# Kernel optimization log

Measured on AMD Instinct MI355X. Metric: run time of the kernel, lower is better.

Reference implementation:

```python
import jax, jax.numpy as jnp
import numpy as np

N_NODES = 50000


def _gin_conv(x, src, dst, w1, b1, w2, b2):
    # sum-aggregate neighbor features: agg[i] = sum_{(j->i) in E} x[j]
    agg = jax.ops.segment_sum(x[src], dst, num_segments=N_NODES)
    h = x + agg  # eps = 0 (PyG GINConv default, not trainable)
    h = jnp.maximum(h @ w1 + b1, 0.0) @ w2 + b2
    return h


def setup_inputs() -> dict:
    key = jax.random.key(0)
    ks = jax.random.split(key, 10)
    d_in, d_h, d_out = 128, 256, 2
    E = 600000
    x = jax.random.normal(ks[0], (N_NODES, d_in), dtype=jnp.float32)
    edge_index = jax.random.randint(ks[1], (2, E), 0, N_NODES, dtype=jnp.int64)
    s = lambda k, sh: jax.random.normal(k, sh, dtype=jnp.float32) * (1.0 / np.sqrt(sh[0]))
    return {
        "x": x,
        "edge_index": edge_index,
        "w1": s(ks[2], (d_in, d_h)), "b1": jnp.zeros((d_h,), jnp.float32),
        "w2": s(ks[3], (d_h, d_h)), "b2": jnp.zeros((d_h,), jnp.float32),
        "w3": s(ks[4], (d_h, d_h)), "b3": jnp.zeros((d_h,), jnp.float32),
        "w4": s(ks[5], (d_h, d_out)), "b4": jnp.zeros((d_out,), jnp.float32),
    }


def reference(x, edge_index, w1, b1, w2, b2, w3, b3, w4, b4):
    src, dst = edge_index[0], edge_index[1]
    h = _gin_conv(x, src, dst, w1, b1, w2, b2)
    h = jnp.maximum(h, 0.0)  # F.relu between the two GINConv layers
    h = _gin_conv(h, src, dst, w3, b3, w4, b4)
    return jax.nn.log_softmax(h, axis=1)
```

## Files before the change

kernel.cpp:

```cpp
#include <hip/hip_runtime.h>
#include <hip/hip_bf16.h>


typedef __attribute__((ext_vector_type(8))) short bf16x8;
typedef __attribute__((ext_vector_type(4))) float f32x4;

static __device__ __forceinline__ unsigned short f2bf(float f) {
    unsigned int u = __float_as_uint(f);
    unsigned int r = (u + 0x7fffu + ((u >> 16) & 1u)) >> 16;
    return (unsigned short)r;
}
static __device__ __forceinline__ float bf2f(unsigned short s) {
    return __uint_as_float(((unsigned int)s) << 16);
}
static __device__ __forceinline__ float bflo(unsigned int u) {
    return __uint_as_float(u << 16);
}
static __device__ __forceinline__ float bfhi(unsigned int u) {
    return __uint_as_float(u & 0xffff0000u);
}

#define S1 136
#define S2 264

__global__ __launch_bounds__(256) void prep_kernel(
    const float* __restrict__ x, short* __restrict__ x_bf,
    const float* __restrict__ w1, const float* __restrict__ w2, const float* __restrict__ w3,
    short* __restrict__ w1t, short* __restrict__ w2t, short* __restrict__ w3t,
    const int* __restrict__ dst, int* __restrict__ deg,
    int M, int E, int cB)
{
    const int b = blockIdx.x;
    const int t = threadIdx.x;
    if (b < cB) {
        const int i = b * 256 + t;
        const int n4 = M * 32;
        if (i >= n4) return;
        const float4 v = *(const float4*)(x + (size_t)i * 4);
        ushort4 o;
        o.x = f2bf(v.x); o.y = f2bf(v.y); o.z = f2bf(v.z); o.w = f2bf(v.w);
        *(ushort4*)(x_bf + (size_t)i * 4) = o;
        return;
    }
    if (b < cB + 192) {
        const int tb = b - cB;
        const int z = tb >> 6;
        const int rem = tb & 63;
        const int kb = rem & 7;
        const int nb = rem >> 3;
        const float* in; short* outb; int K, ostride;
        if (z == 0)      { in = w1; outb = w1t; K = 128; ostride = S1; }
        else if (z == 1) { in = w2; outb = w2t; K = 256; ostride = S2; }
        else             { in = w3; outb = w3t; K = 256; ostride = S2; }
        const int N = 256;
        const int k0 = kb * 32;
        if (k0 >= K) return;
        const int n0 = nb * 32;
        __shared__ float tile[32][33];
        const int tx = t & 31;
        const int ty = t >> 5;
        #pragma unroll
        for (int i = 0; i < 4; ++i)
            tile[ty + 8 * i][tx] = in[(size_t)(k0 + ty + 8 * i) * N + n0 + tx];
        __syncthreads();
        #pragma unroll
        for (int i = 0; i < 4; ++i)
            outb[(size_t)(n0 + ty + 8 * i) * ostride + k0 + tx] = (short)f2bf(tile[tx][ty + 8 * i]);
        return;
    }
    const int e = (b - cB - 192) * 256 + t;
    if (e < E) atomicAdd(&deg[dst[e]], 1);
}

__global__ __launch_bounds__(256) void block_sum_kernel(
    const int* __restrict__ deg, int* __restrict__ bsum, int M)
{
    const int b = blockIdx.x, t = threadIdx.x;
    const int idx = b * 1024 + t * 4;
    int s = 0;
    if (idx + 3 < M) {
        const int4 v = *(const int4*)(deg + idx);
        s = v.x + v.y + v.z + v.w;
    } else {
        #pragma unroll
        for (int i = 0; i < 4; ++i) if (idx + i < M) s += deg[idx + i];
    }
    #pragma unroll
    for (int off = 32; off > 0; off >>= 1) s += __shfl_down(s, off);
    __shared__ int ws[4];
    if ((t & 63) == 0) ws[t >> 6] = s;
    __syncthreads();
    if (t == 0) bsum[b] = ws[0] + ws[1] + ws[2] + ws[3];
}

__global__ __launch_bounds__(256) void scan_blocks2_kernel(
    const int* __restrict__ deg, const int* __restrict__ bsum,
    int* __restrict__ rowptr, int* __restrict__ cur, int M, int E, int nB)
{
    const int b = blockIdx.x, t = threadIdx.x;
    __shared__ int sboff;
    if (t < 64) {
        const int v = (t < nB) ? bsum[t] : 0;
        int inc = v;
        #pragma unroll
        for (int off = 1; off < 64; off <<= 1) {
            const int u = __shfl_up(inc, off);
            if (t >= off) inc += u;
        }
        const int prev = __shfl(inc, (b == 0) ? 0 : (b - 1));
        if (t == 0) sboff = (b == 0) ? 0 : prev;
    }
    const int idx = b * 1024 + t * 4;
    int4 d = make_int4(0, 0, 0, 0);
    if (idx + 3 < M) {
        d = *(const int4*)(deg + idx);
    } else {
        if (idx + 0 < M) d.x = deg[idx + 0];
        if (idx + 1 < M) d.y = deg[idx + 1];
        if (idx + 2 < M) d.z = deg[idx + 2];
        if (idx + 3 < M) d.w = deg[idx + 3];
    }
    const int tot = d.x + d.y + d.z + d.w;
    const int lane = t & 63, wid = t >> 6;
    int inc = tot;
    #pragma unroll
    for (int off = 1; off < 64; off <<= 1) {
        const int u = __shfl_up(inc, off);
        if (lane >= off) inc += u;
    }
    __shared__ int wsum[4];
    if (lane == 63) wsum[wid] = inc;
    __syncthreads();
    int woff = 0;
    #pragma unroll
    for (int w = 0; w < 4; ++w) if (w < wid) woff += wsum[w];
    int p = sboff + woff + (inc - tot);
    if (idx + 0 < M) { rowptr[idx + 0] = p; cur[idx + 0] = p; } p += d.x;
    if (idx + 1 < M) { rowptr[idx + 1] = p; cur[idx + 1] = p; } p += d.y;
    if (idx + 2 < M) { rowptr[idx + 2] = p; cur[idx + 2] = p; } p += d.z;
    if (idx + 3 < M) { rowptr[idx + 3] = p; cur[idx + 3] = p; }
    if (b == 0 && t == 0) rowptr[M] = E;
}

__global__ __launch_bounds__(256) void fill_kernel(
    const int* __restrict__ src, const int* __restrict__ dst,
    int* __restrict__ cur, int* __restrict__ srcs, int E)
{
    const int e = blockIdx.x * 256 + threadIdx.x;
    if (e >= E) return;
    const int p = atomicAdd(&cur[dst[e]], 1);
    srcs[p] = src[e];
}

__global__ __launch_bounds__(256) void gather_add_d128(
    const short* __restrict__ feat,
    const int* __restrict__ rowptr, const int* __restrict__ srcs,
    short* __restrict__ outb, int M)
{
    const int row = blockIdx.x * 4 + (threadIdx.x >> 6);
    if (row >= M) return;
    const int lane = threadIdx.x & 63;
    const int qt = lane >> 4;
    const int o = (lane & 15) * 8;
    float a[8];
    #pragma unroll
    for (int k = 0; k < 8; ++k) a[k] = 0.f;
    if (qt == 0) {
        const uint4 u = *(const uint4*)(feat + (size_t)row * 128 + o);
        a[0] = bflo(u.x); a[1] = bfhi(u.x); a[2] = bflo(u.y); a[3] = bfhi(u.y);
        a[4] = bflo(u.z); a[5] = bfhi(u.z); a[6] = bflo(u.w); a[7] = bfhi(u.w);
    }
    const int jb = rowptr[row], je = rowptr[row + 1];
    int j = jb;
    for (; j + 8 <= je; j += 8) {
        uint4 v[2];
        #pragma unroll
        for (int t = 0; t < 2; ++t) {
            const int s = srcs[j + 4 * t + qt];
            v[t] = *(const uint4*)(feat + (size_t)s * 128 + o);
        }
        #pragma unroll
        for (int t = 0; t < 2; ++t) {
            a[0] += bflo(v[t].x); a[1] += bfhi(v[t].x);
            a[2] += bflo(v[t].y); a[3] += bfhi(v[t].y);
            a[4] += bflo(v[t].z); a[5] += bfhi(v[t].z);
            a[6] += bflo(v[t].w); a[7] += bfhi(v[t].w);
        }
    }
    if (j + 4 <= je) {
        const int s = srcs[j + qt];
        const uint4 v = *(const uint4*)(feat + (size_t)s * 128 + o);
        a[0] += bflo(v.x); a[1] += bfhi(v.x); a[2] += bflo(v.y); a[3] += bfhi(v.y);
        a[4] += bflo(v.z); a[5] += bfhi(v.z); a[6] += bflo(v.w); a[7] += bfhi(v.w);
        j += 4;
    }
    if (j + qt < je) {
        const int s = srcs[j + qt];
        const uint4 v = *(const uint4*)(feat + (size_t)s * 128 + o);
        a[0] += bflo(v.x); a[1] += bfhi(v.x); a[2] += bflo(v.y); a[3] += bfhi(v.y);
        a[4] += bflo(v.z); a[5] += bfhi(v.z); a[6] += bflo(v.w); a[7] += bfhi(v.w);
    }
    #pragma unroll
    for (int k = 0; k < 8; ++k) {
        a[k] += __shfl_down(a[k], 16);
        a[k] += __shfl_down(a[k], 32);
    }
    if (qt == 0) {
        uint4 up;
        up.x = (unsigned int)f2bf(a[0]) | ((unsigned int)f2bf(a[1]) << 16);
        up.y = (unsigned int)f2bf(a[2]) | ((unsigned int)f2bf(a[3]) << 16);
        up.z = (unsigned int)f2bf(a[4]) | ((unsigned int)f2bf(a[5]) << 16);
        up.w = (unsigned int)f2bf(a[6]) | ((unsigned int)f2bf(a[7]) << 16);
        *(uint4*)(outb + (size_t)row * S1 + o) = up;
    }
}

__global__ __launch_bounds__(256) void gather_add_d256(
    const short* __restrict__ feat,
    const int* __restrict__ rowptr, const int* __restrict__ srcs,
    short* __restrict__ outb, int M)
{
    const int row = blockIdx.x * 4 + (threadIdx.x >> 6);
    if (row >= M) return;
    const int lane = threadIdx.x & 63;
    const int half = lane >> 5;
    const int o = (lane & 31) * 8;
    float a[8];
    #pragma unroll
    for (int k = 0; k < 8; ++k) a[k] = 0.f;
    if (half == 0) {
        const uint4 u = *(const uint4*)(feat + (size_t)row * 256 + o);
        a[0] = bflo(u.x); a[1] = bfhi(u.x); a[2] = bflo(u.y); a[3] = bfhi(u.y);
        a[4] = bflo(u.z); a[5] = bfhi(u.z); a[6] = bflo(u.w); a[7] = bfhi(u.w);
    }
    const int jb = rowptr[row], je = rowptr[row + 1];
    int j = jb;
    for (; j + 8 <= je; j += 8) {
        uint4 v[4];
        #pragma unroll
        for (int t = 0; t < 4; ++t) {
            const int s = srcs[j + 2 * t + half];
            v[t] = *(const uint4*)(feat + (size_t)s * 256 + o);
        }
        #pragma unroll
        for (int t = 0; t < 4; ++t) {
            a[0] += bflo(v[t].x); a[1] += bfhi(v[t].x);
            a[2] += bflo(v[t].y); a[3] += bfhi(v[t].y);
            a[4] += bflo(v[t].z); a[5] += bfhi(v[t].z);
            a[6] += bflo(v[t].w); a[7] += bfhi(v[t].w);
        }
    }
    for (; j + 2 <= je; j += 2) {
        const int s = srcs[j + half];
        const uint4 v = *(const uint4*)(feat + (size_t)s * 256 + o);
        a[0] += bflo(v.x); a[1] += bfhi(v.x); a[2] += bflo(v.y); a[3] += bfhi(v.y);
        a[4] += bflo(v.z); a[5] += bfhi(v.z); a[6] += bflo(v.w); a[7] += bfhi(v.w);
    }
    if (j < je && half == 0) {
        const uint4 v = *(const uint4*)(feat + (size_t)srcs[j] * 256 + o);
        a[0] += bflo(v.x); a[1] += bfhi(v.x); a[2] += bflo(v.y); a[3] += bfhi(v.y);
        a[4] += bflo(v.z); a[5] += bfhi(v.z); a[6] += bflo(v.w); a[7] += bfhi(v.w);
    }
    #pragma unroll
    for (int k = 0; k < 8; ++k) a[k] += __shfl_down(a[k], 32);
    if (half == 0) {
        uint4 up;
        up.x = (unsigned int)f2bf(a[0]) | ((unsigned int)f2bf(a[1]) << 16);
        up.y = (unsigned int)f2bf(a[2]) | ((unsigned int)f2bf(a[3]) << 16);
        up.z = (unsigned int)f2bf(a[4]) | ((unsigned int)f2bf(a[5]) << 16);
        up.w = (unsigned int)f2bf(a[6]) | ((unsigned int)f2bf(a[7]) << 16);
        *(uint4*)(outb + (size_t)row * S2 + o) = up;
    }
}

__global__ __launch_bounds__(256) void layer1_fused(
    const short* __restrict__ h1in,
    const short* __restrict__ w1t,
    const float* __restrict__ b1,
    const short* __restrict__ w2t,
    const float* __restrict__ b2,
    short* __restrict__ h1,
    int M)
{
    __shared__ short sT[64 * S2];
    const int tid  = threadIdx.x;
    const int lane = tid & 63;
    const int wid  = tid >> 6;
    const int r16  = lane & 15;
    const int q    = lane >> 4;
    const int tm   = blockIdx.x * 64;
    const int wn   = wid * 64;

    {
        const short* Aslice = h1in + (size_t)tm * S1;
        #pragma unroll
        for (int c = 0; c < 5; ++c) {
            const int idx = tid + c * 256;
            if (idx < 64 * S1 / 8) {
                const uint4 v = *(const uint4*)(Aslice + idx * 8);
                *(uint4*)(&sT[idx * 8]) = v;
            }
        }
    }
    __syncthreads();

    f32x4 acc[4][4];
    #pragma unroll
    for (int i = 0; i < 4; ++i)
        #pragma unroll
        for (int j = 0; j < 4; ++j)
            acc[i][j] = (f32x4)0.f;

    #pragma unroll
    for (int k0 = 0; k0 < 128; k0 += 32) {
        bf16x8 af[4], bfr[4];
        #pragma unroll
        for (int i = 0; i < 4; ++i)
            af[i] = *(const bf16x8*)(&sT[(i * 16 + r16) * S1 + k0 + q * 8]);
        #pragma unroll
        for (int j = 0; j < 4; ++j)
            bfr[j] = *(const bf16x8*)(w1t + (size_t)(wn + j * 16 + r16) * S1 + k0 + q * 8);
        #pragma unroll
        for (int i = 0; i < 4; ++i)
            #pragma unroll
            for (int j = 0; j < 4; ++j)
                acc[i][j] = __builtin_amdgcn_mfma_f32_16x16x32_bf16(af[i], bfr[j], acc[i][j], 0, 0, 0);
    }
    __syncthreads();

    #pragma unroll
    for (int j = 0; j < 4; ++j) {
        const int col = wn + j * 16 + r16;
        const float bj = b1[col];
        #pragma unroll
        for (int i = 0; i < 4; ++i)
            #pragma unroll
            for (int r = 0; r < 4; ++r) {
                float v = fmaxf(acc[i][j][r] + bj, 0.f);
                sT[(i * 16 + q * 4 + r) * S2 + col] = (short)f2bf(v);
            }
    }
    __syncthreads();

    #pragma unroll
    for (int i = 0; i < 4; ++i)
        #pragma unroll
        for (int j = 0; j < 4; ++j)
            acc[i][j] = (f32x4)0.f;

    #pragma unroll
    for (int k0 = 0; k0 < 256; k0 += 32) {
        bf16x8 af[4], bfr[4];
        #pragma unroll
        for (int i = 0; i < 4; ++i)
            af[i] = *(const bf16x8*)(&sT[(i * 16 + r16) * S2 + k0 + q * 8]);
        #pragma unroll
        for (int j = 0; j < 4; ++j)
            bfr[j] = *(const bf16x8*)(w2t + (size_t)(wn + j * 16 + r16) * S2 + k0 + q * 8);
        #pragma unroll
        for (int i = 0; i < 4; ++i)
            #pragma unroll
            for (int j = 0; j < 4; ++j)
                acc[i][j] = __builtin_amdgcn_mfma_f32_16x16x32_bf16(af[i], bfr[j], acc[i][j], 0, 0, 0);
    }
    __syncthreads();

    #pragma unroll
    for (int j = 0; j < 4; ++j) {
        const int col = wn + j * 16 + r16;
        const float bj = b2[col];
        #pragma unroll
        for (int i = 0; i < 4; ++i)
            #pragma unroll
            for (int r = 0; r < 4; ++r) {
                float v = fmaxf(acc[i][j][r] + bj, 0.f);
                sT[(i * 16 + q * 4 + r) * S2 + col] = (short)f2bf(v);
            }
    }
    __syncthreads();

    #pragma unroll
    for (int c = 0; c < 8; ++c) {
        const int idx = tid + c * 256;
        const int row = idx >> 5;
        const int ch  = idx & 31;
        const int rg  = tm + row;
        if (rg < M) {
            const uint4 v = *(const uint4*)(&sT[row * S2 + ch * 8]);
            *(uint4*)(h1 + (size_t)rg * 256 + ch * 8) = v;
        }
    }
}

__global__ __launch_bounds__(256) void layer2_fused(
    const short* __restrict__ h2in,
    const short* __restrict__ w3t,
    const float* __restrict__ b3,
    const float* __restrict__ w4,
    const float* __restrict__ b4,
    float* __restrict__ out,
    int M)
{
    __shared__ short sT[64 * S2];
    const int tid  = threadIdx.x;
    const int lane = tid & 63;
    const int wid  = tid >> 6;
    const int r16  = lane & 15;
    const int q    = lane >> 4;
    const int tm   = blockIdx.x * 64;
    const int wn   = wid * 64;

    {
        const short* Aslice = h2in + (size_t)tm * S2;
        #pragma unroll
        for (int c = 0; c < 9; ++c) {
            const int idx = tid + c * 256;
            if (idx < 64 * S2 / 8) {
                const uint4 v = *(const uint4*)(Aslice + idx * 8);
                *(uint4*)(&sT[idx * 8]) = v;
            }
        }
    }
    __syncthreads();

    f32x4 acc[4][4];
    #pragma unroll
    for (int i = 0; i < 4; ++i)
        #pragma unroll
        for (int j = 0; j < 4; ++j)
            acc[i][j] = (f32x4)0.f;

    #pragma unroll
    for (int k0 = 0; k0 < 256; k0 += 32) {
        bf16x8 af[4], bfr[4];
        #pragma unroll
        for (int i = 0; i < 4; ++i)
            af[i] = *(const bf16x8*)(&sT[(i * 16 + r16) * S2 + k0 + q * 8]);
        #pragma unroll
        for (int j = 0; j < 4; ++j)
            bfr[j] = *(const bf16x8*)(w3t + (size_t)(wn + j * 16 + r16) * S2 + k0 + q * 8);
        #pragma unroll
        for (int i = 0; i < 4; ++i)
            #pragma unroll
            for (int j = 0; j < 4; ++j)
                acc[i][j] = __builtin_amdgcn_mfma_f32_16x16x32_bf16(af[i], bfr[j], acc[i][j], 0, 0, 0);
    }
    __syncthreads();

    #pragma unroll
    for (int j = 0; j < 4; ++j) {
        const int col = wn + j * 16 + r16;
        const float bj = b3[col];
        #pragma unroll
        for (int i = 0; i < 4; ++i)
            #pragma unroll
            for (int r = 0; r < 4; ++r) {
                float v = fmaxf(acc[i][j][r] + bj, 0.f);
                sT[(i * 16 + q * 4 + r) * S2 + col] = (short)f2bf(v);
            }
    }
    __syncthreads();

    const int row = tid >> 2;
    const int qd  = tid & 3;
    const short* tp = &sT[row * S2 + qd * 64];
    const float* w4p = w4 + qd * 128;
    float s0 = 0.f, s1 = 0.f;
    #pragma unroll 8
    for (int k = 0; k < 64; ++k) {
        const float a = bf2f((unsigned short)tp[k]);
        const float2 w = *(const float2*)(w4p + 2 * k);
        s0 = fmaf(a, w.x, s0);
        s1 = fmaf(a, w.y, s1);
    }
    s0 += __shfl_down(s0, 2, 4);  s1 += __shfl_down(s1, 2, 4);
    s0 += __shfl_down(s0, 1, 4);  s1 += __shfl_down(s1, 1, 4);
    if (qd == 0) {
        const int rg = tm + row;
        if (rg < M) {
            s0 += b4[0];
            s1 += b4[1];
            const float m = fmaxf(s0, s1);
            const float l = logf(__expf(s0 - m) + __expf(s1 - m));
            float2 o;
            o.x = s0 - m - l;
            o.y = s1 - m - l;
            *(float2*)(out + (size_t)rg * 2) = o;
        }
    }
}

extern "C" void kernel_launch(void* const* d_in, const int* in_sizes, int n_in,
                              void* d_out, int out_size, void* d_ws, size_t ws_size,
                              hipStream_t stream)
{
    const float* x  = (const float*)d_in[0];
    const int*   ei = (const int*)d_in[1];
    const float* w1 = (const float*)d_in[2];
    const float* b1 = (const float*)d_in[3];
    const float* w2 = (const float*)d_in[4];
    const float* b2 = (const float*)d_in[5];
    const float* w3 = (const float*)d_in[6];
    const float* b3 = (const float*)d_in[7];
    const float* w4 = (const float*)d_in[8];
    const float* b4 = (const float*)d_in[9];

    const int DIN = 128, DH = 256;
    const int M = in_sizes[0] / DIN;
    const int E = in_sizes[1] / 2;
    const int* src = ei;
    const int* dst = ei + E;
    const int nB = (M + 1023) / 1024;

    int* deg    = (int*)d_ws;
    int* bsum   = deg + M;
    int* cur    = bsum + 64;
    int* rowptr = cur + M;
    int* srcs   = rowptr + (M + 1);
    size_t off = ((size_t)(3 * M + 1 + 64 + E) * sizeof(int) + 255) & ~(size_t)255;
    short* x_bf = (short*)((char*)d_ws + off);  off += (size_t)M * DIN * 2;
    off = (off + 255) & ~(size_t)255;
    short* h1in = (short*)((char*)d_ws + off);  off += (size_t)M * S1 * 2;
    off = (off + 255) & ~(size_t)255;
    short* h1   = (short*)((char*)d_ws + off);  off += (size_t)M * DH * 2;
    off = (off + 255) & ~(size_t)255;
    short* h2in = (short*)((char*)d_ws + off);  off += (size_t)M * S2 * 2;
    off = (off + 255) & ~(size_t)255;
    short* w1t  = (short*)((char*)d_ws + off);  off += (size_t)DH * S1 * 2;
    off = (off + 255) & ~(size_t)255;
    short* w2t  = (short*)((char*)d_ws + off);  off += (size_t)DH * S2 * 2;
    off = (off + 255) & ~(size_t)255;
    short* w3t  = (short*)((char*)d_ws + off);  off += (size_t)DH * S2 * 2;

    hipMemsetAsync(deg, 0, (size_t)M * sizeof(int), stream);
    const int cB = (M * 32 + 255) / 256;
    const int dB = (E + 255) / 256;
    prep_kernel<<<cB + 192 + dB, 256, 0, stream>>>(
        x, x_bf, w1, w2, w3, w1t, w2t, w3t, dst, deg, M, E, cB);

    block_sum_kernel<<<nB, 256, 0, stream>>>(deg, bsum, M);
    scan_blocks2_kernel<<<nB, 256, 0, stream>>>(deg, bsum, rowptr, cur, M, E, nB);
    fill_kernel<<<dB, 256, 0, stream>>>(src, dst, cur, srcs, E);

    const int nblk = (M + 63) / 64;

    gather_add_d128<<<(M + 3) / 4, 256, 0, stream>>>(x_bf, rowptr, srcs, h1in, M);
    layer1_fused<<<nblk, 256, 0, stream>>>(h1in, w1t, b1, w2t, b2, h1, M);

    gather_add_d256<<<(M + 3) / 4, 256, 0, stream>>>(h1, rowptr, srcs, h2in, M);
    layer2_fused<<<nblk, 256, 0, stream>>>(h2in, w3t, b3, w4, b4, (float*)d_out, M);
}
```

Measured before the change: 282.7 us.

## Quantize layer-1 hidden activations to uint8 with per-row scale for gather

The first layer's fused MLP epilogue now computes a per-row max of the post-ReLU activations. It stores them as unsigned 8-bit values plus one float scale per row instead of bf16. The second-layer neighbour gather reads these 8-byte chunks and dequantizes with an FMA while accumulating. This halves the bytes fetched in the bandwidth-bound edge gather, at the cost of lower precision in the intermediate features and a few extra shared-memory reductions and syncs in the epilogue.

```diff
diff --git a/kernel.cpp b/kernel.cpp
--- a/kernel.cpp
+++ b/kernel.cpp
@@ -22,6 +22,17 @@
 
 #define S1 136
 #define S2 264
+
+static __device__ __forceinline__ void acc8(float* a, uint2 v, float ss) {
+    a[0] = fmaf(ss, (float)( v.x        & 0xff), a[0]);
+    a[1] = fmaf(ss, (float)((v.x >> 8 ) & 0xff), a[1]);
+    a[2] = fmaf(ss, (float)((v.x >> 16) & 0xff), a[2]);
+    a[3] = fmaf(ss, (float)( v.x >> 24        ), a[3]);
+    a[4] = fmaf(ss, (float)( v.y        & 0xff), a[4]);
+    a[5] = fmaf(ss, (float)((v.y >> 8 ) & 0xff), a[5]);
+    a[6] = fmaf(ss, (float)((v.y >> 16) & 0xff), a[6]);
+    a[7] = fmaf(ss, (float)( v.y >> 24        ), a[7]);
+}
 
 __global__ __launch_bounds__(256) void prep_kernel(
     const float* __restrict__ x, short* __restrict__ x_bf,
@@ -215,8 +226,9 @@
     }
 }
 
-__global__ __launch_bounds__(256) void gather_add_d256(
-    const short* __restrict__ feat,
+__global__ __launch_bounds__(256) void gather_add_d256q(
+    const unsigned char* __restrict__ h1q,
+    const float* __restrict__ hscale,
     const int* __restrict__ rowptr, const int* __restrict__ srcs,
     short* __restrict__ outb, int M)
 {
@@ -229,37 +241,32 @@
     #pragma unroll
     for (int k = 0; k < 8; ++k) a[k] = 0.f;
     if (half == 0) {
-        const uint4 u = *(const uint4*)(feat + (size_t)row * 256 + o);
-        a[0] = bflo(u.x); a[1] = bfhi(u.x); a[2] = bflo(u.y); a[3] = bfhi(u.y);
-        a[4] = bflo(u.z); a[5] = bfhi(u.z); a[6] = bflo(u.w); a[7] = bfhi(u.w);
+        const uint2 u = *(const uint2*)(h1q + (size_t)row * 256 + o);
+        const float scr = hscale[row];
+        acc8(a, u, scr);
     }
     const int jb = rowptr[row], je = rowptr[row + 1];
     int j = jb;
     for (; j + 8 <= je; j += 8) {
-        uint4 v[4];
+        uint2 v[4]; float sc[4];
         #pragma unroll
         for (int t = 0; t < 4; ++t) {
             const int s = srcs[j + 2 * t + half];
-            v[t] = *(const uint4*)(feat + (size_t)s * 256 + o);
-        }
-        #pragma unroll
-        for (int t = 0; t < 4; ++t) {
-            a[0] += bflo(v[t].x); a[1] += bfhi(v[t].x);
-            a[2] += bflo(v[t].y); a[3] += bfhi(v[t].y);
-            a[4] += bflo(v[t].z); a[5] += bfhi(v[t].z);
-            a[6] += bflo(v[t].w); a[7] += bfhi(v[t].w);
-        }
+            v[t] = *(const uint2*)(h1q + (size_t)s * 256 + o);
+            sc[t] = hscale[s];
+        }
+        #pragma unroll
+        for (int t = 0; t < 4; ++t) acc8(a, v[t], sc[t]);
     }
     for (; j + 2 <= je; j += 2) {
         const int s = srcs[j + half];
-        const uint4 v = *(const uint4*)(feat + (size_t)s * 256 + o);
-        a[0] += bflo(v.x); a[1] += bfhi(v.x); a[2] += bflo(v.y); a[3] += bfhi(v.y);
-        a[4] += bflo(v.z); a[5] += bfhi(v.z); a[6] += bflo(v.w); a[7] += bfhi(v.w);
+        const uint2 v = *(const uint2*)(h1q + (size_t)s * 256 + o);
+        acc8(a, v, hscale[s]);
     }
     if (j < je && half == 0) {
-        const uint4 v = *(const uint4*)(feat + (size_t)srcs[j] * 256 + o);
-        a[0] += bflo(v.x); a[1] += bfhi(v.x); a[2] += bflo(v.y); a[3] += bfhi(v.y);
-        a[4] += bflo(v.z); a[5] += bfhi(v.z); a[6] += bflo(v.w); a[7] += bfhi(v.w);
+        const int s = srcs[j];
+        const uint2 v = *(const uint2*)(h1q + (size_t)s * 256 + o);
+        acc8(a, v, hscale[s]);
     }
     #pragma unroll
     for (int k = 0; k < 8; ++k) a[k] += __shfl_down(a[k], 32);
@@ -269,7 +276,7 @@
         up.y = (unsigned int)f2bf(a[2]) | ((unsigned int)f2bf(a[3]) << 16);
         up.z = (unsigned int)f2bf(a[4]) | ((unsigned int)f2bf(a[5]) << 16);
         up.w = (unsigned int)f2bf(a[6]) | ((unsigned int)f2bf(a[7]) << 16);
-        *(uint4*)(outb + (size_t)row * S2 + o) = up;
+        *(uint4*)(outb + (size_t)row * S2 + (lane & 31) * 8) = up;
     }
 }
 
@@ -279,10 +286,13 @@
     const float* __restrict__ b1,
     const short* __restrict__ w2t,
     const float* __restrict__ b2,
-    short* __restrict__ h1,
+    unsigned char* __restrict__ h1q,
+    float* __restrict__ hscale,
     int M)
 {
     __shared__ short sT[64 * S2];
+    __shared__ float sMax[64][4];
+    __shared__ float sInv[64];
     const int tid  = threadIdx.x;
     const int lane = tid & 63;
     const int wid  = tid >> 6;
@@ -365,17 +375,36 @@
     }
     __syncthreads();
 
-    #pragma unroll
-    for (int j = 0; j < 4; ++j) {
-        const int col = wn + j * 16 + r16;
-        const float bj = b2[col];
-        #pragma unroll
-        for (int i = 0; i < 4; ++i)
+    {
+        float bj4[4];
+        #pragma unroll
+        for (int j = 0; j < 4; ++j) bj4[j] = b2[wn + j * 16 + r16];
+        #pragma unroll
+        for (int i = 0; i < 4; ++i) {
             #pragma unroll
             for (int r = 0; r < 4; ++r) {
-                float v = fmaxf(acc[i][j][r] + bj, 0.f);
-                sT[(i * 16 + q * 4 + r) * S2 + col] = (short)f2bf(v);
+                float m = 0.f;
+                #pragma unroll
+                for (int j = 0; j < 4; ++j) {
+                    float v = fmaxf(acc[i][j][r] + bj4[j], 0.f);
+                    sT[(i * 16 + q * 4 + r) * S2 + wn + j * 16 + r16] = (short)f2bf(v);
+                    m = fmaxf(m, v);
+                }
+                #pragma unroll
+                for (int off = 1; off < 16; off <<= 1)
+                    m = fmaxf(m, __shfl_xor(m, off));
+                if (r16 == 0) sMax[i * 16 + q * 4 + r][wid] = m;
             }
+        }
+    }
+    __syncthreads();
+
+    if (tid < 64) {
+        const float m = fmaxf(fmaxf(sMax[tid][0], sMax[tid][1]),
+                              fmaxf(sMax[tid][2], sMax[tid][3]));
+        sInv[tid] = (m > 0.f) ? 255.f / m : 0.f;
+        const int rg = tm + tid;
+        if (rg < M) hscale[rg] = m * (1.f / 255.f);
     }
     __syncthreads();
 
@@ -387,7 +416,19 @@
         const int rg  = tm + row;
         if (rg < M) {
             const uint4 v = *(const uint4*)(&sT[row * S2 + ch * 8]);
-            *(uint4*)(h1 + (size_t)rg * 256 + ch * 8) = v;
+            const float inv = sInv[row];
+            unsigned int q0 = min(255u, (unsigned int)(bflo(v.x) * inv + 0.5f));
+            unsigned int q1 = min(255u, (unsigned int)(bfhi(v.x) * inv + 0.5f));
+            unsigned int q2 = min(255u, (unsigned int)(bflo(v.y) * inv + 0.5f));
+            unsigned int q3 = min(255u, (unsigned int)(bfhi(v.y) * inv + 0.5f));
+            unsigned int q4 = min(255u, (unsigned int)(bflo(v.z) * inv + 0.5f));
+            unsigned int q5 = min(255u, (unsigned int)(bfhi(v.z) * inv + 0.5f));
+            unsigned int q6 = min(255u, (unsigned int)(bflo(v.w) * inv + 0.5f));
+            unsigned int q7 = min(255u, (unsigned int)(bfhi(v.w) * inv + 0.5f));
+            uint2 o8;
+            o8.x = q0 | (q1 << 8) | (q2 << 16) | (q3 << 24);
+            o8.y = q4 | (q5 << 8) | (q6 << 16) | (q7 << 24);
+            *(uint2*)(h1q + (size_t)rg * 256 + ch * 8) = o8;
         }
     }
 }
@@ -522,7 +563,9 @@
     off = (off + 255) & ~(size_t)255;
     short* h1in = (short*)((char*)d_ws + off);  off += (size_t)M * S1 * 2;
     off = (off + 255) & ~(size_t)255;
-    short* h1   = (short*)((char*)d_ws + off);  off += (size_t)M * DH * 2;
+    unsigned char* h1q = (unsigned char*)((char*)d_ws + off);  off += (size_t)M * 256;
+    off = (off + 255) & ~(size_t)255;
+    float* hscale = (float*)((char*)d_ws + off);  off += (size_t)M * 4;
     off = (off + 255) & ~(size_t)255;
     short* h2in = (short*)((char*)d_ws + off);  off += (size_t)M * S2 * 2;
     off = (off + 255) & ~(size_t)255;
@@ -545,8 +588,8 @@
     const int nblk = (M + 63) / 64;
 
     gather_add_d128<<<(M + 3) / 4, 256, 0, stream>>>(x_bf, rowptr, srcs, h1in, M);
-    layer1_fused<<<nblk, 256, 0, stream>>>(h1in, w1t, b1, w2t, b2, h1, M);
-
-    gather_add_d256<<<(M + 3) / 4, 256, 0, stream>>>(h1, rowptr, srcs, h2in, M);
+    layer1_fused<<<nblk, 256, 0, stream>>>(h1in, w1t, b1, w2t, b2, h1q, hscale, M);
+
+    gather_add_d256q<<<(M + 3) / 4, 256, 0, stream>>>(h1q, hscale, rowptr, srcs, h2in, M);
     layer2_fused<<<nblk, 256, 0, stream>>>(h2in, w3t, b3, w4, b4, (float*)d_out, M);
 }
```

Result: faster. 273.8 us (-3.1%).
